# Optimization experiments

Measured on AMD Instinct MI355X. Metric: run time of the kernel, lower is better.

Reference implementation:

```python
import jax, jax.numpy as jnp
import numpy as np
from math import factorial, pi

# ---- network constants (hard-coded in s2net.__init__) ----
B_IN, B1, B2 = 15, 10, 6
F1, F2, F_OUT = 20, 40, 10
M1, C1 = 2 * B1 - 1, B1 - 1   # 19, 9
M2, C2 = 2 * B2 - 1, B2 - 1   # 11, 5


def _wigner_d(l, beta):
    # Wigner small-d matrix d^l_{m,n}(beta), quantum convention. [2l+1, 2l+1]
    d = np.zeros((2 * l + 1, 2 * l + 1))
    cb, sb = np.cos(beta / 2.0), np.sin(beta / 2.0)
    for mi, m in enumerate(range(-l, l + 1)):
        for ni, n in enumerate(range(-l, l + 1)):
            pref = np.sqrt(float(factorial(l + m) * factorial(l - m) * factorial(l + n) * factorial(l - n)))
            v = 0.0
            for s in range(max(0, n - m), min(l + n, l - m) + 1):
                v += ((-1.0) ** (m - n + s)
                      / (factorial(l + n - s) * factorial(s) * factorial(m - n + s) * factorial(l - m - s))
                      * cb ** (2 * l + n - m - 2 * s) * sb ** (m - n + 2 * s))
            d[mi, ni] = pref * v
    return d


def _wigner_stack(betas, nl):
    # zero-padded stack [n_beta, nl, 2nl-1, 2nl-1], centered at nl-1
    M, c = 2 * nl - 1, nl - 1
    W = np.zeros((len(betas), nl, M, M))
    for k, beta in enumerate(betas):
        for l in range(nl):
            W[k, l, c - l:c + l + 1, c - l:c + l + 1] = _wigner_d(l, beta)
    return W


def _quad_weights(b):
    # Driscoll-Healy quadrature weights at beta_k = pi(2k+1)/(4b)
    k = np.arange(2 * b)
    beta = pi * (2 * k + 1) / (4 * b)
    j = np.arange(b)
    return (2.0 / b) * np.sin(beta) * (np.sin((2 * j[None] + 1) * beta[:, None]) / (2 * j + 1)).sum(1)


# ---- precomputed spectral constants (numpy, once) ----
_betas_in = pi * (2 * np.arange(2 * B_IN) + 1) / (4 * B_IN)
_w_in = _quad_weights(B_IN)
W_S2_FWD = jnp.asarray((_wigner_stack(_betas_in, B1)[:, :, :, C1] * _w_in[:, None, None]).astype(np.float32))  # [30,10,19]
M_IDX1 = jnp.asarray(np.arange(-C1, C1 + 1) % (2 * B_IN))

# s2 near-identity grid (max_beta=pi/8, n_alpha=8, n_beta=3) -> 24 pts
_g_beta = np.arange(1, 4) * (pi / 8) / 3
_g_alpha = np.linspace(0, 2 * pi, 8, endpoint=False)
_grid_s2 = [(b, a) for b in _g_beta for a in _g_alpha]
_bs2 = np.zeros((len(_grid_s2), B1, M1), np.complex64)
for _p, (_bt, _al) in enumerate(_grid_s2):
    for _l in range(B1):
        _bs2[_p, _l, C1 - _l:C1 + _l + 1] = _wigner_d(_l, _bt)[:, _l] * np.exp(-1j * np.arange(-_l, _l + 1) * _al)
B_S2 = jnp.asarray(_bs2)

_betas1 = pi * (2 * np.arange(2 * B1) + 1) / (4 * B1)
_scale1 = (2 * np.arange(B1) + 1).astype(np.float64)
W_INV1 = jnp.asarray((_wigner_stack(_betas1, B1) * _scale1[None, :, None, None]).astype(np.float32))  # [20,10,19,19]
_a1 = 2 * pi * np.arange(2 * B1) / (2 * B1)
E_A1 = jnp.asarray(np.exp(1j * np.arange(-C1, C1 + 1)[:, None] * _a1[None, :]).astype(np.complex64))  # [19,20]
E_G1 = E_A1

_w1 = _quad_weights(B1)
W_SO3_FWD = jnp.asarray((_wigner_stack(_betas1, B2) * _w1[:, None, None, None]).astype(np.float32))  # [20,6,11,11]
M_IDX2 = jnp.asarray(np.arange(-C2, C2 + 1) % (2 * B1))

# so3 near-identity grid (8 alphas x 3 betas x 6 gammas) -> 144 pts
_g_gamma = np.linspace(0, 2 * pi, 6, endpoint=False)
_grid_so3 = [(b, a, g) for b in _g_beta for a in _g_alpha for g in _g_gamma]
_bso3 = np.zeros((len(_grid_so3), B2, M2, M2), np.complex64)
for _p, (_bt, _al, _ga) in enumerate(_grid_so3):
    for _l in range(B2):
        _em = np.exp(-1j * np.arange(-_l, _l + 1) * _al)
        _eg = np.exp(-1j * np.arange(-_l, _l + 1) * _ga)
        _bso3[_p, _l, C2 - _l:C2 + _l + 1, C2 - _l:C2 + _l + 1] = _wigner_d(_l, _bt) * _em[:, None] * _eg[None, :]
B_SO3 = jnp.asarray(_bso3)

_betas2 = pi * (2 * np.arange(2 * B2) + 1) / (4 * B2)
_scale2 = (2 * np.arange(B2) + 1).astype(np.float64)
W_INV2 = jnp.asarray((_wigner_stack(_betas2, B2) * _scale2[None, :, None, None]).astype(np.float32))  # [12,6,11,11]
_a2 = 2 * pi * np.arange(2 * B2) / (2 * B2)
E_A2 = jnp.asarray(np.exp(1j * np.arange(-C2, C2 + 1)[:, None] * _a2[None, :]).astype(np.complex64))  # [11,12]
E_G2 = E_A2
W_INT = jnp.asarray(_quad_weights(B2).astype(np.float32))  # [12]


def setup_inputs() -> dict:
    key = jax.random.key(0)
    ks = jax.random.split(key, 4)
    x = jax.random.normal(ks[0], (128, 1, 2 * B_IN, 2 * B_IN), jnp.float32)
    kernel1 = jax.random.normal(ks[1], (1, F1, 24), jnp.float32) * 0.2
    kernel2 = jax.random.normal(ks[2], (F1, F2, 144), jnp.float32) * 0.05
    w_lin = jax.random.normal(ks[3], (F_OUT, F2), jnp.float32) * 0.1
    b_lin = jnp.zeros((F_OUT,), jnp.float32)
    return {"x": x, "kernel1": kernel1, "kernel2": kernel2, "w_lin": w_lin, "b_lin": b_lin}


def reference(x, kernel1, kernel2, w_lin, b_lin):
    # ---- S2 convolution: b_in=15 -> b_out=10 ----
    xf = jnp.fft.fft(x.astype(jnp.complex64), axis=-1)            # FFT over alpha
    xm = xf[..., M_IDX1]                                          # [B,1,30,19] m=-9..9
    X = jnp.einsum('klm,bckm->bclm', W_S2_FWD, xm)                # S2 FFT -> [B,1,10,19]
    psi = jnp.einsum('iop,plm->iolm', kernel1.astype(jnp.complex64), B_S2)
    Z = jnp.einsum('bilm,ioln->bolmn', X, jnp.conj(psi))          # s2_mm -> [B,20,10,19,19]
    fh = jnp.einsum('klmn,bolmn->bokmn', W_INV1, Z)               # [B,20,20,19,19]
    y = jnp.einsum('bokmn,ma,ng->bokag', fh, E_A1, E_G1).real     # SO3 iFFT -> [B,20,20,20,20]
    y = jax.nn.relu(y)
    # ---- SO3 convolution: b=10 -> b=6 ----
    yf = jnp.fft.fft2(y.astype(jnp.complex64), axes=(-2, -1))     # FFT over alpha,gamma
    ymn = yf[..., M_IDX2[:, None], M_IDX2[None, :]]               # [B,20,20,11,11]
    X2 = jnp.einsum('klmn,bckmn->bclmn', W_SO3_FWD, ymn)          # SO3 FFT -> [B,20,6,11,11]
    psi2 = jnp.einsum('iop,plmn->iolmn', kernel2.astype(jnp.complex64), B_SO3)
    Z2 = jnp.einsum('bilmk,iolnk->bolmn', X2, jnp.conj(psi2))     # so3_mm -> [B,40,6,11,11]
    fh2 = jnp.einsum('klmn,bolmn->bokmn', W_INV2, Z2)             # [B,40,12,11,11]
    y2 = jnp.einsum('bokmn,ma,ng->bokag', fh2, E_A2, E_G2).real   # [B,40,12,12,12]
    y2 = jax.nn.relu(y2)
    # ---- so3_integrate + linear head ----
    feat = jnp.einsum('bokag,k->bo', y2, W_INT) / float((2 * B2) ** 2)  # [B,40]
    return feat @ w_lin.T + b_lin
```

## Files before the change

### kernel.cpp

```cpp
#include <hip/hip_runtime.h>
#include <math.h>


constexpr int OFF_WS2   = 0;
constexpr int OFF_WINV1 = OFF_WS2   + 5700;
constexpr int OFF_WSO3  = OFF_WINV1 + 72200;
constexpr int OFF_WINV2 = OFF_WSO3  + 14520;
constexpr int OFF_WINT  = OFF_WINV2 + 8712;
constexpr int OFF_FE1   = OFF_WINT  + 16;
constexpr int OFF_EA1   = OFF_FE1   + 1140;
constexpr int OFF_FF2   = OFF_EA1   + 760;
constexpr int OFF_EA2   = OFF_FF2   + 440;
constexpr int OFF_BS2   = OFF_EA2   + 264;
constexpr int OFF_BSO3  = OFF_BS2   + 9120;
constexpr int OFF_PSI   = OFF_BSO3  + 209088;
constexpr int OFF_X     = OFF_PSI   + 7600;
constexpr int OFF_X2P   = OFF_X     + 48640;
constexpr int OFF_PSI2P = OFF_X2P   + 1464320;
constexpr int OFF_FEAT  = OFF_PSI2P + 457600;
constexpr int OFF_VTAB  = OFF_FEAT  + 20480;
constexpr int OFF_VTAB2 = OFF_VTAB  + 286;
constexpr int OFF_ZMAP  = OFF_VTAB2 + 146;

#define DPI 3.14159265358979323846

__device__ __forceinline__ double dfact(int n) {
    double f = 1.0;
    for (int i = 2; i <= n; ++i) f *= (double)i;
    return f;
}
__device__ __forceinline__ double dpowi(double x, int n) {
    double r = 1.0;
    for (int i = 0; i < n; ++i) r *= x;
    return r;
}
__device__ double wig_d(int l, int mi, int ni, double beta) {
    int m = mi - l, n = ni - l;
    double cb = cos(0.5 * beta), sb = sin(0.5 * beta);
    double pref = sqrt(dfact(l + m) * dfact(l - m) * dfact(l + n) * dfact(l - n));
    int s0 = (n - m) > 0 ? (n - m) : 0;
    int s1 = (l + n) < (l - m) ? (l + n) : (l - m);
    double v = 0.0;
    for (int s = s0; s <= s1; ++s) {
        double term = dpowi(cb, 2 * l + n - m - 2 * s) * dpowi(sb, m - n + 2 * s) /
                      (dfact(l + n - s) * dfact(s) * dfact(m - n + s) * dfact(l - m - s));
        v += ((m - n + s) & 1) ? -term : term;
    }
    return pref * v;
}
__device__ double wig_pad(int l, int m, int n, int c, double beta) {
    if (m < c - l || m > c + l || n < c - l || n > c + l) return 0.0;
    return wig_d(l, m - (c - l), n - (c - l), beta);
}
__device__ double quad_w(int b, int k) {
    double beta = DPI * (2 * k + 1) / (4.0 * b);
    double s = 0.0;
    for (int j = 0; j < b; ++j) s += sin((2 * j + 1) * beta) / (double)(2 * j + 1);
    return 2.0 / b * sin(beta) * s;
}

__global__ __launch_bounds__(256) void build_tables_kernel(float* ws) {
    int idx = blockIdx.x * 256 + threadIdx.x;
    if (idx < 5700) {
        int k = idx / 190, r = idx % 190, l = r / 19, m = r % 19;
        double beta = DPI * (2 * k + 1) / 60.0;
        ws[OFF_WS2 + idx] = (float)(quad_w(15, k) * wig_pad(l, m, 9, 9, beta));
        return;
    }
    idx -= 5700;
    if (idx < 72200) {
        int k = idx / 3610, r = idx % 3610, l = r / 361, r2 = r % 361, m = r2 / 19, n = r2 % 19;
        if (m < 9) return;
        double beta = DPI * (2 * k + 1) / 40.0;
        ws[OFF_WINV1 + idx] = (float)((2 * l + 1) * wig_pad(l, m, n, 9, beta));
        return;
    }
    idx -= 72200;
    if (idx < 14520) {
        int k = idx / 726, r = idx % 726, l = r / 121, m = (r % 121) / 11, n = r % 11;
        double beta = DPI * (2 * k + 1) / 40.0;
        ws[OFF_WSO3 + idx] = (float)(quad_w(10, k) * wig_pad(l, m, n, 5, beta));
        return;
    }
    idx -= 14520;
    if (idx < 8712) {
        int k = idx / 726, r = idx % 726, l = r / 121, m = (r % 121) / 11, n = r % 11;
        if (m < 5) return;
        double beta = DPI * (2 * k + 1) / 24.0;
        ws[OFF_WINV2 + idx] = (float)((2 * l + 1) * wig_pad(l, m, n, 5, beta));
        return;
    }
    idx -= 8712;
    if (idx < 12) { ws[OFF_WINT + idx] = (float)quad_w(6, idx); return; }
    idx -= 12;
    if (idx < 570) {
        int m = idx / 30, t = idx % 30;
        double ang = -2.0 * DPI * (double)((m - 9) * t) / 30.0;
        ws[OFF_FE1 + 2 * idx] = (float)cos(ang);
        ws[OFF_FE1 + 2 * idx + 1] = (float)sin(ang);
        return;
    }
    idx -= 570;
    if (idx < 380) {
        int m = idx / 20, a = idx % 20;
        double ang = 2.0 * DPI * (double)((m - 9) * a) / 20.0;
        ws[OFF_EA1 + 2 * idx] = (float)cos(ang);
        ws[OFF_EA1 + 2 * idx + 1] = (float)sin(ang);
        return;
    }
    idx -= 380;
    if (idx < 220) {
        int m = idx / 20, a = idx % 20;
        double ang = -2.0 * DPI * (double)((m - 5) * a) / 20.0;
        ws[OFF_FF2 + 2 * idx] = (float)cos(ang);
        ws[OFF_FF2 + 2 * idx + 1] = (float)sin(ang);
        return;
    }
    idx -= 220;
    if (idx < 132) {
        int m = idx / 12, a = idx % 12;
        double ang = 2.0 * DPI * (double)((m - 5) * a) / 12.0;
        ws[OFF_EA2 + 2 * idx] = (float)cos(ang);
        ws[OFF_EA2 + 2 * idx + 1] = (float)sin(ang);
        return;
    }
    idx -= 132;
    if (idx < 4560) {
        int p = idx / 190, r = idx % 190, l = r / 19, m = r % 19;
        int bi = p / 8, ai = p % 8;
        double beta = (bi + 1) * (DPI / 24.0);
        double alpha = 2.0 * DPI * ai / 8.0;
        double re = 0.0, im = 0.0;
        if (m - 9 >= -l && m - 9 <= l) {
            double d = wig_d(l, m - 9 + l, l, beta);
            double ang = -(double)(m - 9) * alpha;
            re = d * cos(ang); im = d * sin(ang);
        }
        ws[OFF_BS2 + 2 * idx] = (float)re;
        ws[OFF_BS2 + 2 * idx + 1] = (float)im;
        return;
    }
    idx -= 4560;
    if (idx < 104544) {
        int p = idx / 726, r = idx % 726, l = r / 121, m = (r % 121) / 11, n = r % 11;
        int dm = m - 5, dn = n - 5;
        int am = dm < 0 ? -dm : dm, an = dn < 0 ? -dn : dn;
        if (am > l || an > l) return;
        if (!((dm > 0) || (dm == 0 && dn >= 0))) return;
        int bi = p / 48, ai = (p % 48) / 6, gi = p % 6;
        double beta = (bi + 1) * (DPI / 24.0);
        double alpha = 2.0 * DPI * ai / 8.0;
        double gamma = 2.0 * DPI * gi / 6.0;
        double d = wig_d(l, m - 5 + l, n - 5 + l, beta);
        double ang = -((double)(m - 5) * alpha + (double)(n - 5) * gamma);
        ws[OFF_BSO3 + 2 * idx] = (float)(d * cos(ang));
        ws[OFF_BSO3 + 2 * idx + 1] = (float)(d * sin(ang));
        return;
    }
    idx -= 104544;
    if (idx < 286) {
        int l = 0, cum = 0;
        while (idx >= cum + (2 * l + 1) * (2 * l + 1)) { cum += (2 * l + 1) * (2 * l + 1); ++l; }
        int rem = idx - cum, w = 2 * l + 1;
        int m = 5 - l + rem / w, n = 5 - l + rem % w;
        ((int*)(ws + OFF_VTAB))[idx] = l | (m << 4) | (n << 8);
        return;
    }
    idx -= 286;
    if (idx < 146) {
        int l = 5, st = 0;
        while (idx >= st + (2 * l * l + 2 * l + 1)) { st += 2 * l * l + 2 * l + 1; --l; }
        int rem = idx - st;
        int dm, dn;
        if (rem < l + 1) { dm = 0; dn = rem; }
        else { int r2 = rem - (l + 1); dm = 1 + r2 / (2 * l + 1); dn = r2 % (2 * l + 1) - l; }
        ((int*)(ws + OFF_VTAB2))[idx] = l | ((dm + 5) << 4) | ((dn + 5) << 8);
        return;
    }
    idx -= 146;
    if (idx < 396) {
        int ll = idx / 66, rr = idx - ll * 66, dm = rr / 11, n = rr - dm * 11;
        int dn = n - 5, an = dn < 0 ? -dn : dn;
        int zv = -1;
        if (dm <= ll && an <= ll) {
            bool inhalf = (dm > 0) || (dm == 0 && dn >= 0);
            int ddm = inhalf ? dm : -dm, ddn = inhalf ? dn : -dn;
            int lp = ll + 1;
            int st = 146 - lp * (2 * lp * lp + 1) / 3;
            int h = st + (ddm == 0 ? ddn : (ll + 1) + (ddm - 1) * (2 * ll + 1) + (ddn + ll));
            zv = h;
            if (!inhalf) zv |= 256 | ((((dm + an) & 1) ? 1 : 0) << 9);
        }
        ((int*)(ws + OFF_ZMAP))[idx] = zv;
        return;
    }
}

__global__ __launch_bounds__(256) void prep_kernel(float* ws,
                                                   const float* __restrict__ k1,
                                                   const float* __restrict__ k2,
                                                   const float* __restrict__ x) {
    const int bid = blockIdx.x, tid = threadIdx.x;
    __shared__ float xs[900];
    __shared__ float2 xm[570];

    if (bid < 457) {
        int idx = bid * 256 + tid;
        if (idx >= 116800) return;
        int i = idx / 5840, r = idx % 5840, o = r / 146, h = r % 146;
        int w = ((const int*)(ws + OFF_VTAB2))[h];
        int l = w & 15, dm = ((w >> 4) & 15) - 5, dn = ((w >> 8) & 15) - 5;
        int lmn = l * 121 + (dm + 5) * 11 + (dn + 5);
        const float2* BS = (const float2*)(ws + OFF_BSO3);
        float2 s = {0.f, 0.f};
        for (int p = 0; p < 144; ++p) {
            float wv = k2[(i * 40 + o) * 144 + p];
            float2 bv = BS[p * 726 + lmn];
            s.x += wv * bv.x; s.y += wv * bv.y;
        }
        float2* row = (float2*)(ws + OFF_PSI2P) + (i * 40 + o) * 286;
        int base = l * (4 * l * l - 1) / 3, span = 2 * l + 1;
        row[base + (dm + l) * span + (dn + l)] = s;
        float sign = ((dm + dn + 16) & 1) ? -1.f : 1.f;
        row[base + (-dm + l) * span + (-dn + l)] = make_float2(sign * s.x, -sign * s.y);
        return;
    }
    if (bid < 585) {
        const int b = bid - 457;
        const float2* FE1 = (const float2*)(ws + OFF_FE1);
        const float* WS2 = ws + OFF_WS2;
        float2* Xg = (float2*)(ws + OFF_X) + b * 190;
        for (int i = tid; i < 900; i += 256) xs[i] = x[b * 900 + i];
        __syncthreads();
        for (int i = tid; i < 570; i += 256) {
            int k = i / 19, m = i % 19;
            float2 s = {0.f, 0.f};
            #pragma unroll
            for (int t = 0; t < 30; ++t) {
                float v = xs[k * 30 + t];
                float2 e = FE1[m * 30 + t];
                s.x += v * e.x; s.y += v * e.y;
            }
            xm[k * 19 + m] = s;
        }
        __syncthreads();
        for (int i = tid; i < 190; i += 256) {
            int l = i / 19, m = i % 19;
            float2 s = {0.f, 0.f};
            for (int k = 0; k < 30; ++k) {
                float w = WS2[k * 190 + l * 19 + m];
                float2 v = xm[k * 19 + m];
                s.x += w * v.x; s.y += w * v.y;
            }
            Xg[i] = s;
        }
        return;
    }
    {
        int idx = (bid - 585) * 256 + tid;
        if (idx >= 3800) return;
        int o = idx / 190, r = idx % 190;
        const float2* BS2 = (const float2*)(ws + OFF_BS2);
        float2 s = {0.f, 0.f};
        for (int p = 0; p < 24; ++p) {
            float w = k1[o * 24 + p];
            float2 bv = BS2[p * 190 + r];
            s.x += w * bv.x; s.y += w * bv.y;
        }
        ((float2*)(ws + OFF_PSI))[idx] = s;
    }
}

__global__ __launch_bounds__(256, 4) void stage1_kernel(
    const float* __restrict__ WI1, const float* __restrict__ WS3,
    const float* __restrict__ EA1, const float* __restrict__ FF2,
    const float2* __restrict__ Xall, const float2* __restrict__ Pall,
    const int* __restrict__ VTAB, float2* __restrict__ X2out)
{
    const int tid = threadIdx.x;
    const int b = blockIdx.x / 20;
    const int o = blockIdx.x % 20;
    const float2* Xg = Xall + b * 190;
    const float2* Pg = Pall + o * 190;
    float2* X2g = X2out + (b * 20 + o) * 286;
    const float2* EA1c = (const float2*)EA1;
    const float2* FF2c = (const float2*)FF2;

    __shared__ float2 Xs[190], Ps[190], FF2s[220];
    __shared__ float2 fhA[3800];
    float2* const ymnA = fhA + 2400;

    const int gpair = tid % 10;
    const int kk = tid / 10;
    const bool active = (tid < 200);

    float2 eg[19];
    #pragma unroll
    for (int n = 0; n < 19; ++n) eg[n] = EA1c[n * 20 + gpair];

    for (int i = tid; i < 190; i += 256) { Xs[i] = Xg[i]; Ps[i] = Pg[i]; }
    for (int i = tid; i < 220; i += 256) FF2s[i] = FF2c[i];
    __syncthreads();

    for (int i = tid; i < 3800; i += 256) {
        int k = i / 190, idx = i - k * 190;
        int mrow = idx / 19, ni = idx - mrow * 19;
        int mi = mrow + 9;
        int an = ni > 9 ? ni - 9 : 9 - ni;
        int lmin = mrow > an ? mrow : an;
        const float* wk = WI1 + k * 3610 + mi * 19 + ni;
        float2 s = {0.f, 0.f};
        for (int l = lmin; l < 10; ++l) {
            float2 a = Xs[l * 19 + mi], c = Ps[l * 19 + ni];
            float wv = wk[l * 361];
            s.x += wv * (a.x * c.x + a.y * c.y);
            s.y += wv * (a.y * c.x - a.x * c.y);
        }
        fhA[i] = s;
    }
    __syncthreads();

    float2 uacc0[6], uacc1[6];
    if (active) {
        const float2* fhk = fhA + kk * 190;
        float ye0[10], yo0[10], ye1[10], yo1[10];
        {
            float2 te = {0.f, 0.f}, to = {0.f, 0.f};
            #pragma unroll
            for (int n = 0; n < 19; ++n) {
                float2 f = fhk[n];
                float rx = f.x * eg[n].x - f.y * eg[n].y;
                float ry = f.x * eg[n].y + f.y * eg[n].x;
                if (n & 1) { te.x += rx; te.y += ry; }
                else       { to.x += rx; to.y += ry; }
            }
            float t0x = te.x + to.x, t1x = te.x - to.x;
            #pragma unroll
            for (int a = 0; a < 10; ++a) {
                ye0[a] = t0x; yo0[a] = 0.f;
                ye1[a] = t1x; yo1[a] = 0.f;
            }
        }
        #pragma unroll 1
        for (int mrow = 1; mrow < 10; ++mrow) {
            float2 te = {0.f, 0.f}, to = {0.f, 0.f};
            #pragma unroll
            for (int n = 0; n < 19; ++n) {
                float2 f = fhk[mrow * 19 + n];
                float rx = f.x * eg[n].x - f.y * eg[n].y;
                float ry = f.x * eg[n].y + f.y * eg[n].x;
                if (n & 1) { te.x += rx; te.y += ry; }
                else       { to.x += rx; to.y += ry; }
            }
            float2 t0 = make_float2(2.f * (te.x + to.x), 2.f * (te.y + to.y));
            float2 t1 = make_float2(2.f * (te.x - to.x), 2.f * (te.y - to.y));
            if (mrow & 1) {
                #pragma unroll
                for (int a = 0; a < 10; ++a) {
                    float2 e = EA1c[(9 + mrow) * 20 + a];
                    yo0[a] += t0.x * e.x - t0.y * e.y;
                    yo1[a] += t1.x * e.x - t1.y * e.y;
                }
            } else {
                #pragma unroll
                for (int a = 0; a < 10; ++a) {
                    float2 e = EA1c[(9 + mrow) * 20 + a];
                    ye0[a] += t0.x * e.x - t0.y * e.y;
                    ye1[a] += t1.x * e.x - t1.y * e.y;
                }
            }
        }
        #pragma unroll
        for (int a = 0; a < 10; ++a) {
            float p0 = ye0[a] + yo0[a]; p0 = p0 > 0.f ? p0 : 0.f;
            float q0 = ye0[a] - yo0[a]; q0 = q0 > 0.f ? q0 : 0.f;
            ye0[a] = p0 + q0; yo0[a] = p0 - q0;
            float p1 = ye1[a] + yo1[a]; p1 = p1 > 0.f ? p1 : 0.f;
            float q1 = ye1[a] - yo1[a]; q1 = q1 > 0.f ? q1 : 0.f;
            ye1[a] = p1 + q1; yo1[a] = p1 - q1;
        }
        uacc0[0] = make_float2(0.f, 0.f); uacc1[0] = make_float2(0.f, 0.f);
        #pragma unroll
        for (int a = 0; a < 10; ++a) { uacc0[0].x += ye0[a]; uacc1[0].x += ye1[a]; }
        #pragma unroll
        for (int d = 1; d < 6; ++d) {
            uacc0[d] = make_float2(0.f, 0.f); uacc1[d] = make_float2(0.f, 0.f);
            #pragma unroll
            for (int a = 0; a < 10; ++a) {
                float q0 = (d & 1) ? yo0[a] : ye0[a];
                float q1 = (d & 1) ? yo1[a] : ye1[a];
                float2 e = FF2c[(5 + d) * 20 + a];
                uacc0[d].x += e.x * q0; uacc0[d].y += e.y * q0;
                uacc1[d].x += e.x * q1; uacc1[d].y += e.y * q1;
            }
        }
    }
    __syncthreads();

    float2* uubuf = fhA;
    if (active) {
        #pragma unroll
        for (int d = 0; d < 6; ++d) {
            uubuf[kk * 120 + d * 20 + gpair]      = uacc0[d];
            uubuf[kk * 120 + d * 20 + gpair + 10] = uacc1[d];
        }
    }
    __syncthreads();

    for (int i = tid; i < 1320; i += 256) {
        int k = i / 66, rr = i - k * 66;
        int d = rr / 11, ni = rr - d * 11;
        const float2* uurow = uubuf + k * 120 + d * 20;
        float sgn = (ni & 1) ? 1.f : -1.f;
        float2 s = {0.f, 0.f};
        #pragma unroll
        for (int gg = 0; gg < 10; ++gg) {
            float2 ua = uurow[gg], ub = uurow[gg + 10];
            float ux = ua.x + sgn * ub.x, uy = ua.y + sgn * ub.y;
            float2 e = FF2s[ni * 20 + gg];
            s.x += ux * e.x - uy * e.y;
            s.y += ux * e.y + uy * e.x;
        }
        ymnA[i] = s;
    }
    __syncthreads();

    for (int v = tid; v < 286; v += 256) {
        int w = VTAB[v];
        int l = w & 15, m = (w >> 4) & 15, n = (w >> 8) & 15;
        int fidx = l * 121 + m * 11 + n;
        int off; float sy;
        if (m >= 5) { off = (m - 5) * 11 + n; sy = 1.f; }
        else        { off = (5 - m) * 11 + (10 - n); sy = -1.f; }
        float2 s = {0.f, 0.f};
        for (int k = 0; k < 20; ++k) {
            float wv = WS3[k * 726 + fidx];
            float2 ym = ymnA[k * 66 + off];
            s.x += wv * ym.x;
            s.y += wv * sy * ym.y;
        }
        X2g[v] = s;
    }
}

__global__ __launch_bounds__(256) void stage2_kernel(float* ws) {
    const int tid = threadIdx.x;
    const int wave = tid >> 6, lane = tid & 63;
    const int bp = blockIdx.x / 20;
    const int og = blockIdx.x % 20;
    const int b0 = bp * 2, o0 = og * 2;
    const int bsel = wave >> 1, osel = wave & 1;

    const float*  WI2 = ws + OFF_WINV2;
    const float2* EA2 = (const float2*)(ws + OFF_EA2);
    const float*  WIT = ws + OFF_WINT;
    const int*  VTAB2 = (const int*)(ws + OFF_VTAB2);
    const int*   ZMAP = (const int*)(ws + OFF_ZMAP);
    const float4* WS4 = (const float4*)ws;
    float* featp = ws + OFF_FEAT;

    __shared__ __align__(16) float sm[5744];

    int xo[3], po[3], klen[3];
    float2 acc[3];
    #pragma unroll
    for (int t = 0; t < 3; ++t) {
        int v = lane + 64 * t;
        acc[t] = make_float2(0.f, 0.f);
        if (v < 146) {
            int w = VTAB2[v];
            int l = w & 15, dm = ((w >> 4) & 15) - 5, dn = ((w >> 8) & 15) - 5;
            int base = l * (4 * l * l - 1) / 3, span = 2 * l + 1;
            xo[t] = base + (dm + l) * span;
            po[t] = base + (dn + l) * span;
            klen[t] = span;
        } else { xo[t] = 0; po[t] = 0; klen[t] = 0; }
    }

    int fb[3], fstep[3];
    #pragma unroll
    for (int j = 0; j < 3; ++j) {
        int v = tid + 256 * j;
        fb[j] = 0; fstep[j] = 0;
        if (v < 572) {
            int arr = v / 143, idx = v - arr * 143;
            if (arr < 2) { fb[j] = (OFF_X2P >> 2) + (b0 + arr) * 20 * 143 + idx; fstep[j] = 143; }
            else         { fb[j] = (OFF_PSI2P >> 2) + (o0 + arr - 2) * 143 + idx; fstep[j] = 5720; }
        }
    }
    const bool f2ok = (tid < 60);

    float4 rg0 = WS4[fb[0]];
    float4 rg1 = WS4[fb[1]];
    float4 rg2;
    if (f2ok) rg2 = WS4[fb[2]];

    for (int i = 0; i < 20; ++i) {
        float4* B4 = (float4*)(sm + 1168 + (i & 1) * 2288);
        B4[tid]       = rg0;
        B4[tid + 256] = rg1;
        if (f2ok) B4[tid + 512] = rg2;
        __syncthreads();
        if (i + 1 < 20) {
            rg0 = WS4[fb[0] + (i + 1) * fstep[0]];
            rg1 = WS4[fb[1] + (i + 1) * fstep[1]];
            if (f2ok) rg2 = WS4[fb[2] + (i + 1) * fstep[2]];
        }
        const float2* bufF2 = (const float2*)(sm + 1168 + (i & 1) * 2288);
        const float2* xiW = bufF2 + bsel * 286;
        const float2* ppW = bufF2 + (2 + osel) * 286;
        #pragma unroll
        for (int t = 0; t < 3; ++t) {
            for (int k = 0; k < klen[t]; ++k) {
                float2 u = xiW[xo[t] + k], v2 = ppW[po[t] + k];
                acc[t].x += u.x * v2.x + u.y * v2.y;
                acc[t].y += u.y * v2.x - u.x * v2.y;
            }
        }
    }

    float2* P = (float2*)sm;
    #pragma unroll
    for (int t = 0; t < 3; ++t) {
        int v = lane + 64 * t;
        if (v < 146) P[wave * 146 + v] = acc[t];
    }
    __syncthreads();

    float2* z2s = (float2*)(sm + 1168);
    float2* fh2 = (float2*)(sm + 1960);
    float2* t2  = (float2*)(sm + 3544);
    for (int p = 0; p < 4; ++p) {
        for (int idx = tid; idx < 396; idx += 256) {
            int zv = ZMAP[idx];
            float2 s = {0.f, 0.f};
            if (zv >= 0) {
                s = P[p * 146 + (zv & 255)];
                if (zv & 256) {
                    float sg = (zv & 512) ? -1.f : 1.f;
                    s = make_float2(sg * s.x, -sg * s.y);
                }
            }
            z2s[idx] = s;
        }
        __syncthreads();
        for (int li = lane; li < 198; li += 64) {
            int k2 = wave * 3 + li / 66;
            int rr = li % 66;
            int mrow = rr / 11, n = rr - mrow * 11;
            int dn = n - 5, an = dn < 0 ? -dn : dn;
            int lmin = mrow > an ? mrow : an;
            int mfull = mrow + 5;
            float2 s = {0.f, 0.f};
            for (int ll = lmin; ll < 6; ++ll) {
                float w = WI2[k2 * 726 + ll * 121 + mfull * 11 + n];
                float2 z = z2s[ll * 66 + mrow * 11 + n];
                s.x += w * z.x; s.y += w * z.y;
            }
            fh2[k2 * 66 + rr] = s;
        }
        asm volatile("s_waitcnt lgkmcnt(0)" ::: "memory");
        for (int li = lane; li < 216; li += 64) {
            int k2 = wave * 3 + li / 72;
            int rr = li % 72, mrow = rr / 12, g = rr - mrow * 12;
            float2 s = {0.f, 0.f};
            #pragma unroll
            for (int n = 0; n < 11; ++n) {
                float2 f = fh2[k2 * 66 + mrow * 11 + n], e = EA2[n * 12 + g];
                s.x += f.x * e.x - f.y * e.y;
                s.y += f.x * e.y + f.y * e.x;
            }
            t2[k2 * 72 + rr] = s;
        }
        asm volatile("s_waitcnt lgkmcnt(0)" ::: "memory");
        float partial = 0.f;
        for (int li = lane; li < 216; li += 64) {
            int k2 = wave * 3 + li / 72;
            int rr = li % 72, a = rr / 12, g = rr - a * 12;
            float base = t2[k2 * 72 + g].x;
            float se = 0.f, so = 0.f;
            #pragma unroll
            for (int d = 1; d < 6; ++d) {
                float2 e = EA2[(5 + d) * 12 + a];
                float2 t = t2[k2 * 72 + d * 12 + g];
                float c = 2.f * (e.x * t.x - e.y * t.y);
                if (d & 1) so += c; else se += c;
            }
            float y0 = base + se + so, y1 = base + se - so;
            float w = WIT[k2];
            if (y0 > 0.f) partial += w * y0;
            if (y1 > 0.f) partial += w * y1;
        }
        for (int off = 32; off > 0; off >>= 1) partial += __shfl_down(partial, off, 64);
        if (lane == 0)
            featp[((b0 + (p >> 1)) * 40 + o0 + (p & 1)) * 4 + wave] = partial;
        __syncthreads();
    }
}

__global__ __launch_bounds__(256) void final_kernel(const float* __restrict__ ws,
                                                    const float* __restrict__ wl,
                                                    const float* __restrict__ bl,
                                                    float* __restrict__ out) {
    int idx = blockIdx.x * 256 + threadIdx.x;
    if (idx >= 1280) return;
    int b = idx / 10, f = idx % 10;
    const float* fp = ws + OFF_FEAT;
    float s = bl[f];
    for (int o = 0; o < 40; ++o) {
        const float* q = fp + (b * 40 + o) * 4;
        s += ((q[0] + q[1] + q[2] + q[3]) * (1.0f / 144.0f)) * wl[f * 40 + o];
    }
    out[idx] = s;
}

extern "C" void kernel_launch(void* const* d_in, const int* in_sizes, int n_in,
                              void* d_out, int out_size, void* d_ws, size_t ws_size,
                              hipStream_t stream) {
    (void)in_sizes; (void)n_in; (void)out_size; (void)ws_size;
    const float* x  = (const float*)d_in[0];
    const float* k1 = (const float*)d_in[1];
    const float* k2 = (const float*)d_in[2];
    const float* wl = (const float*)d_in[3];
    const float* bl = (const float*)d_in[4];
    float* out = (float*)d_out;
    float* ws  = (float*)d_ws;

    build_tables_kernel<<<830, 256, 0, stream>>>(ws);
    prep_kernel<<<600, 256, 0, stream>>>(ws, k1, k2, x);
    stage1_kernel<<<128 * 20, 256, 0, stream>>>(
        ws + OFF_WINV1, ws + OFF_WSO3, ws + OFF_EA1, ws + OFF_FF2,
        (const float2*)(ws + OFF_X), (const float2*)(ws + OFF_PSI),
        (const int*)(ws + OFF_VTAB), (float2*)(ws + OFF_X2P));
    stage2_kernel<<<128 * 10, 256, 0, stream>>>(ws);
    final_kernel<<<5, 256, 0, stream>>>(ws, wl, bl, out);
}
```

Measured before the change: 304.7 us.

## Fully unroll stage2 contraction loops, double-buffer z2 staging, and tabulate factorials

```diff
diff --git a/kernel.cpp b/kernel.cpp
--- a/kernel.cpp
+++ b/kernel.cpp
@@ -24,33 +24,28 @@
 
 #define DPI 3.14159265358979323846
 
-__device__ __forceinline__ double dfact(int n) {
-    double f = 1.0;
-    for (int i = 2; i <= n; ++i) f *= (double)i;
-    return f;
-}
 __device__ __forceinline__ double dpowi(double x, int n) {
     double r = 1.0;
     for (int i = 0; i < n; ++i) r *= x;
     return r;
 }
-__device__ double wig_d(int l, int mi, int ni, double beta) {
+__device__ double wig_d(const double* F, int l, int mi, int ni, double beta) {
     int m = mi - l, n = ni - l;
     double cb = cos(0.5 * beta), sb = sin(0.5 * beta);
-    double pref = sqrt(dfact(l + m) * dfact(l - m) * dfact(l + n) * dfact(l - n));
+    double pref = sqrt(F[l + m] * F[l - m] * F[l + n] * F[l - n]);
     int s0 = (n - m) > 0 ? (n - m) : 0;
     int s1 = (l + n) < (l - m) ? (l + n) : (l - m);
     double v = 0.0;
     for (int s = s0; s <= s1; ++s) {
         double term = dpowi(cb, 2 * l + n - m - 2 * s) * dpowi(sb, m - n + 2 * s) /
-                      (dfact(l + n - s) * dfact(s) * dfact(m - n + s) * dfact(l - m - s));
+                      (F[l + n - s] * F[s] * F[m - n + s] * F[l - m - s]);
         v += ((m - n + s) & 1) ? -term : term;
     }
     return pref * v;
 }
-__device__ double wig_pad(int l, int m, int n, int c, double beta) {
+__device__ double wig_pad(const double* F, int l, int m, int n, int c, double beta) {
     if (m < c - l || m > c + l || n < c - l || n > c + l) return 0.0;
-    return wig_d(l, m - (c - l), n - (c - l), beta);
+    return wig_d(F, l, m - (c - l), n - (c - l), beta);
 }
 __device__ double quad_w(int b, int k) {
     double beta = DPI * (2 * k + 1) / (4.0 * b);
@@ -60,11 +55,20 @@
 }
 
 __global__ __launch_bounds__(256) void build_tables_kernel(float* ws) {
+    __shared__ double sfact[21];
+    if (threadIdx.x == 0) {
+        double f = 1.0;
+        sfact[0] = 1.0;
+        for (int i = 1; i <= 20; ++i) { f *= (double)i; sfact[i] = f; }
+    }
+    __syncthreads();
+    const double* F = sfact;
+
     int idx = blockIdx.x * 256 + threadIdx.x;
     if (idx < 5700) {
         int k = idx / 190, r = idx % 190, l = r / 19, m = r % 19;
         double beta = DPI * (2 * k + 1) / 60.0;
-        ws[OFF_WS2 + idx] = (float)(quad_w(15, k) * wig_pad(l, m, 9, 9, beta));
+        ws[OFF_WS2 + idx] = (float)(quad_w(15, k) * wig_pad(F, l, m, 9, 9, beta));
         return;
     }
     idx -= 5700;
@@ -72,14 +76,14 @@
         int k = idx / 3610, r = idx % 3610, l = r / 361, r2 = r % 361, m = r2 / 19, n = r2 % 19;
         if (m < 9) return;
         double beta = DPI * (2 * k + 1) / 40.0;
-        ws[OFF_WINV1 + idx] = (float)((2 * l + 1) * wig_pad(l, m, n, 9, beta));
+        ws[OFF_WINV1 + idx] = (float)((2 * l + 1) * wig_pad(F, l, m, n, 9, beta));
         return;
     }
     idx -= 72200;
     if (idx < 14520) {
         int k = idx / 726, r = idx % 726, l = r / 121, m = (r % 121) / 11, n = r % 11;
         double beta = DPI * (2 * k + 1) / 40.0;
-        ws[OFF_WSO3 + idx] = (float)(quad_w(10, k) * wig_pad(l, m, n, 5, beta));
+        ws[OFF_WSO3 + idx] = (float)(quad_w(10, k) * wig_pad(F, l, m, n, 5, beta));
         return;
     }
     idx -= 14520;
@@ -87,7 +91,7 @@
         int k = idx / 726, r = idx % 726, l = r / 121, m = (r % 121) / 11, n = r % 11;
         if (m < 5) return;
         double beta = DPI * (2 * k + 1) / 24.0;
-        ws[OFF_WINV2 + idx] = (float)((2 * l + 1) * wig_pad(l, m, n, 5, beta));
+        ws[OFF_WINV2 + idx] = (float)((2 * l + 1) * wig_pad(F, l, m, n, 5, beta));
         return;
     }
     idx -= 8712;
@@ -132,7 +136,7 @@
         double alpha = 2.0 * DPI * ai / 8.0;
         double re = 0.0, im = 0.0;
         if (m - 9 >= -l && m - 9 <= l) {
-            double d = wig_d(l, m - 9 + l, l, beta);
+            double d = wig_d(F, l, m - 9 + l, l, beta);
             double ang = -(double)(m - 9) * alpha;
             re = d * cos(ang); im = d * sin(ang);
         }
@@ -151,7 +155,7 @@
         double beta = (bi + 1) * (DPI / 24.0);
         double alpha = 2.0 * DPI * ai / 8.0;
         double gamma = 2.0 * DPI * gi / 6.0;
-        double d = wig_d(l, m - 5 + l, n - 5 + l, beta);
+        double d = wig_d(F, l, m - 5 + l, n - 5 + l, beta);
         double ang = -((double)(m - 5) * alpha + (double)(n - 5) * gamma);
         ws[OFF_BSO3 + 2 * idx] = (float)(d * cos(ang));
         ws[OFF_BSO3 + 2 * idx + 1] = (float)(d * sin(ang));
@@ -459,7 +463,7 @@
     const float4* WS4 = (const float4*)ws;
     float* featp = ws + OFF_FEAT;
 
-    __shared__ __align__(16) float sm[5744];
+    __shared__ __align__(16) float sm[6064];
 
     int xo[3], po[3], klen[3];
     float2 acc[3];
@@ -495,26 +499,59 @@
     float4 rg2;
     if (f2ok) rg2 = WS4[fb[2]];
 
+    constexpr int KMAX0 = 11, KMAX1 = 9, KMAX2 = 5;
     for (int i = 0; i < 20; ++i) {
-        float4* B4 = (float4*)(sm + 1168 + (i & 1) * 2288);
+        float4* B4 = (float4*)(sm + 1168 + (i & 1) * 2320);
         B4[tid]       = rg0;
         B4[tid + 256] = rg1;
         if (f2ok) B4[tid + 512] = rg2;
         __syncthreads();
         if (i + 1 < 20) {
-            rg0 = WS4[fb[0] + (i + 1) * fstep[0]];
-            rg1 = WS4[fb[1] + (i + 1) * fstep[1]];
-            if (f2ok) rg2 = WS4[fb[2] + (i + 1) * fstep[2]];
-        }
-        const float2* bufF2 = (const float2*)(sm + 1168 + (i & 1) * 2288);
+            fb[0] += fstep[0]; fb[1] += fstep[1]; fb[2] += fstep[2];
+            rg0 = WS4[fb[0]];
+            rg1 = WS4[fb[1]];
+            if (f2ok) rg2 = WS4[fb[2]];
+        }
+        const float2* bufF2 = (const float2*)(sm + 1168 + (i & 1) * 2320);
         const float2* xiW = bufF2 + bsel * 286;
         const float2* ppW = bufF2 + (2 + osel) * 286;
-        #pragma unroll
-        for (int t = 0; t < 3; ++t) {
-            for (int k = 0; k < klen[t]; ++k) {
-                float2 u = xiW[xo[t] + k], v2 = ppW[po[t] + k];
-                acc[t].x += u.x * v2.x + u.y * v2.y;
-                acc[t].y += u.y * v2.x - u.x * v2.y;
+        {
+            const float2* xp = xiW + xo[0];
+            const float2* pq = ppW + po[0];
+            const int kl = klen[0];
+            #pragma unroll
+            for (int k = 0; k < KMAX0; ++k) {
+                float2 u = xp[k], v2 = pq[k];
+                if (k < kl) {
+                    acc[0].x += u.x * v2.x + u.y * v2.y;
+                    acc[0].y += u.y * v2.x - u.x * v2.y;
+                }
+            }
+        }
+        {
+            const float2* xp = xiW + xo[1];
+            const float2* pq = ppW + po[1];
+            const int kl = klen[1];
+            #pragma unroll
+            for (int k = 0; k < KMAX1; ++k) {
+                float2 u = xp[k], v2 = pq[k];
+                if (k < kl) {
+                    acc[1].x += u.x * v2.x + u.y * v2.y;
+                    acc[1].y += u.y * v2.x - u.x * v2.y;
+                }
+            }
+        }
+        {
+            const float2* xp = xiW + xo[2];
+            const float2* pq = ppW + po[2];
+            const int kl = klen[2];
+            #pragma unroll
+            for (int k = 0; k < KMAX2; ++k) {
+                float2 u = xp[k], v2 = pq[k];
+                if (k < kl) {
+                    acc[2].x += u.x * v2.x + u.y * v2.y;
+                    acc[2].y += u.y * v2.x - u.x * v2.y;
+                }
             }
         }
     }
@@ -527,23 +564,28 @@
     }
     __syncthreads();
 
-    float2* z2s = (float2*)(sm + 1168);
-    float2* fh2 = (float2*)(sm + 1960);
-    float2* t2  = (float2*)(sm + 3544);
+    float2* z2A = (float2*)(sm + 1168);
+    float2* z2B = (float2*)(sm + 1960);
+    float2* fh2 = (float2*)(sm + 2752);
+    float2* t2  = (float2*)(sm + 4336);
+
+    for (int idx = tid; idx < 396; idx += 256) {
+        int zv = ZMAP[idx];
+        float2 s = {0.f, 0.f};
+        if (zv >= 0) {
+            s = P[(zv & 255)];
+            if (zv & 256) {
+                float sg = (zv & 512) ? -1.f : 1.f;
+                s = make_float2(sg * s.x, -sg * s.y);
+            }
+        }
+        z2A[idx] = s;
+    }
+    __syncthreads();
+
     for (int p = 0; p < 4; ++p) {
-        for (int idx = tid; idx < 396; idx += 256) {
-            int zv = ZMAP[idx];
-            float2 s = {0.f, 0.f};
-            if (zv >= 0) {
-                s = P[p * 146 + (zv & 255)];
-                if (zv & 256) {
-                    float sg = (zv & 512) ? -1.f : 1.f;
-                    s = make_float2(sg * s.x, -sg * s.y);
-                }
-            }
-            z2s[idx] = s;
-        }
-        __syncthreads();
+        const float2* zin  = (p & 1) ? z2B : z2A;
+        float2*       zout = (p & 1) ? z2A : z2B;
         for (int li = lane; li < 198; li += 64) {
             int k2 = wave * 3 + li / 66;
             int rr = li % 66;
@@ -554,12 +596,26 @@
             float2 s = {0.f, 0.f};
             for (int ll = lmin; ll < 6; ++ll) {
                 float w = WI2[k2 * 726 + ll * 121 + mfull * 11 + n];
-                float2 z = z2s[ll * 66 + mrow * 11 + n];
+                float2 z = zin[ll * 66 + mrow * 11 + n];
                 s.x += w * z.x; s.y += w * z.y;
             }
             fh2[k2 * 66 + rr] = s;
         }
         asm volatile("s_waitcnt lgkmcnt(0)" ::: "memory");
+        if (p < 3) {
+            for (int idx = tid; idx < 396; idx += 256) {
+                int zv = ZMAP[idx];
+                float2 s = {0.f, 0.f};
+                if (zv >= 0) {
+                    s = P[(p + 1) * 146 + (zv & 255)];
+                    if (zv & 256) {
+                        float sg = (zv & 512) ? -1.f : 1.f;
+                        s = make_float2(sg * s.x, -sg * s.y);
+                    }
+                }
+                zout[idx] = s;
+            }
+        }
         for (int li = lane; li < 216; li += 64) {
             int k2 = wave * 3 + li / 72;
             int rr = li % 72, mrow = rr / 12, g = rr - mrow * 12;
```

New measurement: 277.7 us. 1.1x faster.
